# Kernel tuning notes

Hardware: AMD Instinct MI355X
Metric: run time of the kernel (lower is better)

## Reference

```python
import jax, jax.numpy as jnp
import numpy as np

B, N, D, H = 2, 2048, 1024, 16
HD = D // H
SCALE = HD ** -0.5


def setup_inputs() -> dict:
    key = jax.random.key(0)
    ks = jax.random.split(key, 5)
    s = 0.02
    return {
        "x": jax.random.normal(ks[0], (B, N, D), dtype=jnp.float32),
        "Wq": jax.random.normal(ks[1], (D, D), dtype=jnp.float32) * s,
        "Wk": jax.random.normal(ks[2], (D, D), dtype=jnp.float32) * s,
        "Wv": jax.random.normal(ks[3], (D, D), dtype=jnp.float32) * s,
        "Wo": jax.random.normal(ks[4], (D, D), dtype=jnp.float32) * s,
        "bo": jnp.zeros((D,), dtype=jnp.float32),
    }


def reference(x, Wq, Wk, Wv, Wo, bo):
    # Q/K/V projections (torch Linear: y = x @ W.T), bias-free
    q = jnp.einsum("bnd,ed->bne", x, Wq)
    k = jnp.einsum("bnd,ed->bne", x, Wk)
    v = jnp.einsum("bnd,ed->bne", x, Wv)
    # split heads: (b, n, h*d) -> (b, h, n, d)
    split = lambda t: t.reshape(B, N, H, HD).transpose(0, 2, 1, 3)
    q, k, v = split(q), split(k), split(v)
    # full attention matrix, softmax over keys
    sim = jnp.einsum("bhnd,bhmd->bhnm", q, k) * SCALE
    attn = jax.nn.softmax(sim, axis=-1)
    out = jnp.einsum("bhnm,bhmd->bhnd", attn, v)
    out = out.transpose(0, 2, 1, 3).reshape(B, N, D)
    return jnp.einsum("bnd,ed->bne", out, Wo) + bo
```

## Files before the change

### kernel.cpp

```cpp
#include <hip/hip_runtime.h>
#include <hip/hip_bf16.h>
#include <stdint.h>

#define B_ 2
#define N_ 2048
#define D_ 1024
#define H_ 16
#define SCALE_L2E 0.18033688011112042f

typedef unsigned short u16;
typedef unsigned int u32;
using f32x4  = __attribute__((ext_vector_type(4))) float;
using f32x16 = __attribute__((ext_vector_type(16))) float;
using bf16x8 = __attribute__((ext_vector_type(8))) short;
using i16x8  = __attribute__((ext_vector_type(8))) short;

__device__ __forceinline__ u16 f2b(float f) {
  unsigned u = __float_as_uint(f);
  return (u16)((u + 0x7FFFu + ((u >> 16) & 1u)) >> 16);
}
__device__ __forceinline__ u32 pk2(float lo, float hi) {
  u32 r;
  asm("v_cvt_pk_bf16_f32 %0, %1, %2" : "=v"(r) : "v"(lo), "v"(hi));
  return r;
}
__device__ __forceinline__ float ex2(float x) {
  return __builtin_amdgcn_exp2f(x);
}
__device__ __forceinline__ void async16(const u16* g, u16* l) {
  __builtin_amdgcn_global_load_lds(
      (const __attribute__((address_space(1))) void*)g,
      (__attribute__((address_space(3))) void*)l, 16, 0, 0);
}
__device__ __forceinline__ void cfence() {
  asm volatile("" ::: "memory");
  __builtin_amdgcn_sched_barrier(0);
}

__global__ __launch_bounds__(256) void cast_all(
    const float* __restrict__ x, const float* __restrict__ w0,
    const float* __restrict__ w1, const float* __restrict__ w2,
    const float* __restrict__ w3, u16* __restrict__ xb, u16* __restrict__ Wb) {
  const int i = (blockIdx.x * 256 + threadIdx.x) * 8;
  const float* s;
  u16* d;
  if (i < 4194304) { s = x + i; d = xb + i; }
  else {
    const int j = i - 4194304;
    const int wsel = j >> 20;
    const float* w = wsel == 0 ? w0 : wsel == 1 ? w1 : wsel == 2 ? w2 : w3;
    s = w + (j & 1048575);
    d = Wb + j;
  }
  union { u32 u[4]; i16x8 v; } o;
#pragma unroll
  for (int j = 0; j < 4; ++j) o.u[j] = pk2(s[2 * j], s[2 * j + 1]);
  *(i16x8*)d = o.v;
}

template <int F32OUT>
__global__ __launch_bounds__(256) void gemm_bt(
    const u16* __restrict__ A, const u16* __restrict__ Bt,
    void* __restrict__ C0, size_t sCz, const float* __restrict__ bias,
    int M, int Nn, int K) {
  __shared__ __align__(16) u16 As[128 * 64];
  __shared__ __align__(16) u16 Bs[64 * 64];
  const int tid = threadIdx.x;
  const int w = tid >> 6, l = tid & 63;
  const int wm = w >> 1, wn = w & 1;
  const int la = l & 15, lb = l >> 4;
  const int tM = blockIdx.y * 128, tN = blockIdx.x * 64;

  const int srow8 = l >> 3;
  const int scol  = ((l & 7) ^ srow8) << 3;
  const u16* gA = A + (size_t)(tM + w * 32 + srow8) * K + scol;
  const u16* gB = Bt + (size_t)(tN + w * 16 + srow8) * K + scol;
  u16* lA = As + w * 2048;
  u16* lB = Bs + w * 1024;

  f32x4 acc[4][2] = {};

  for (int k0 = 0; k0 < K; k0 += 64) {
#pragma unroll
    for (int c = 0; c < 4; ++c)
      async16(gA + (size_t)(c * 8) * K, lA + c * 512);
#pragma unroll
    for (int c = 0; c < 2; ++c)
      async16(gB + (size_t)(c * 8) * K, lB + c * 512);
    gA += 64; gB += 64;
    __syncthreads();
    bf16x8 af[4][2], bfr[2][2];
#pragma unroll
    for (int i = 0; i < 4; ++i) {
      const int row = wm * 64 + i * 16 + la;
#pragma unroll
      for (int kk = 0; kk < 2; ++kk)
        af[i][kk] = *(const bf16x8*)(As + row * 64 + (((kk * 4 + lb) ^ (row & 7)) << 3));
    }
#pragma unroll
    for (int j = 0; j < 2; ++j) {
      const int row = wn * 32 + j * 16 + la;
#pragma unroll
      for (int kk = 0; kk < 2; ++kk)
        bfr[j][kk] = *(const bf16x8*)(Bs + row * 64 + (((kk * 4 + lb) ^ (row & 7)) << 3));
    }
#pragma unroll
    for (int kk = 0; kk < 2; ++kk)
#pragma unroll
      for (int i = 0; i < 4; ++i)
#pragma unroll
        for (int j = 0; j < 2; ++j)
          acc[i][j] = __builtin_amdgcn_mfma_f32_16x16x32_bf16(
              af[i][kk], bfr[j][kk], acc[i][j], 0, 0, 0);
    __syncthreads();
  }

  const int zsel = F32OUT ? 0 : (tN >> 10);
  const int tNl = F32OUT ? tN : (tN & 1023);
  const float osc = (!F32OUT && zsel == 0) ? SCALE_L2E : 1.0f;
  const int ld = F32OUT ? Nn : 1024;
#pragma unroll
  for (int i = 0; i < 4; ++i) {
    const int row = tM + wm * 64 + i * 16 + lb * 4;
#pragma unroll
    for (int j = 0; j < 2; ++j) {
      const int col = tNl + wn * 32 + j * 16 + la;
#pragma unroll
      for (int r = 0; r < 4; ++r) {
        const float v = acc[i][j][r];
        if (F32OUT) {
          ((float*)C0)[(size_t)(row + r) * ld + col] = v + bias[col];
        } else {
          (((u16*)C0) + (size_t)zsel * sCz)[(size_t)(row + r) * ld + col] = f2b(v * osc);
        }
      }
    }
  }
}

__global__ __launch_bounds__(256) void vtrans(const u16* __restrict__ V,
                                              u16* __restrict__ Vt) {
  __shared__ u16 T[64][72];
  const int tid = threadIdx.x;
  const int rt = blockIdx.x, h = blockIdx.y;
  const int r = tid >> 3, c = (tid & 7) * 8;
#pragma unroll
  for (int p = 0; p < 2; ++p) {
    i16x8 v = *(const i16x8*)(V + (size_t)(rt * 64 + p * 32 + r) * D_ + h * 64 + c);
#pragma unroll
    for (int j = 0; j < 8; ++j) T[p * 32 + r][c + j] = (u16)v[j];
  }
  __syncthreads();
  const int b = rt >> 5, nb = (rt & 31) * 64;
#pragma unroll
  for (int p = 0; p < 2; ++p) {
    const int d = p * 32 + r;
    i16x8 o;
#pragma unroll
    for (int j = 0; j < 8; ++j) o[j] = (short)T[c + j][d];
    *(i16x8*)(Vt + ((size_t)((b * 16 + h) * 64 + d)) * (size_t)N_ + nb + c) = o;
  }
}

__global__ __launch_bounds__(256) void attn_fused(
    const u16* __restrict__ Q, const u16* __restrict__ Kb,
    const u16* __restrict__ VtG, u16* __restrict__ O) {
  __shared__ __align__(16) u16 Ks[2 * 64 * 64];
  __shared__ __align__(16) u16 Vs[2 * 64 * 64];
  const int tid = threadIdx.x;
  const int w = tid >> 6, l = tid & 63;
  const int q = l & 31, hi = l >> 5;

  const int flat = blockIdx.x + 16 * blockIdx.y;
  const int logical = (flat & 7) * 64 + (flat >> 3);
  const int qx = logical & 15;
  const int y  = logical >> 4;

  const int b = y >> 4, h = y & 15;
  const int q0 = qx * 128 + w * 32;

  const u16* Qrow = Q + (size_t)(b * N_ + q0 + q) * D_ + h * 64;
  bf16x8 qf[4];
#pragma unroll
  for (int s = 0; s < 4; ++s) qf[s] = *(const bf16x8*)(Qrow + s * 16 + hi * 8);

  const int srow = l >> 3;
  const int scol = ((l & 7) ^ srow) << 3;
  const int kprow = w * 16 + (srow & 3) + ((srow & 4) << 1);
  const u16* Kg = Kb + (size_t)(b * N_ + kprow) * D_ + h * 64 + scol;
  const u16* Vg = VtG + (size_t)(y * 64 + w * 16 + srow) * N_ + scol;

  const int qsw = (q & 7) << 3;
  const int qr0 = q * 64, qr1 = (32 + q) * 64;

  union { u32 u[4]; bf16x8 v; } ones;
#pragma unroll
  for (int j = 0; j < 4; ++j) ones.u[j] = 0x3F803F80u;

  f32x16 o0 = {}, o1 = {}, o_l = {};

  auto stage = [&](int t, int buf) {
    const u16* kg = Kg + (size_t)(t * 64) * D_;
    u16* kd = Ks + buf * 4096 + w * 1024;
    async16(kg, kd);
    async16(kg + (size_t)4 * D_, kd + 512);
    const u16* vg = Vg + t * 64;
    u16* vd = Vs + buf * 4096 + w * 1024;
    async16(vg, vd);
    async16(vg + (size_t)8 * N_, vd + 512);
  };

  const int NT = N_ / 64;
  stage(0, 0);
  stage(1, 1);

  for (int t = 0; t < NT; ++t) {
    const int buf = t & 1;
    if (t + 1 < NT) asm volatile("s_waitcnt vmcnt(4)" ::: "memory");
    else            asm volatile("s_waitcnt vmcnt(0)" ::: "memory");
    __builtin_amdgcn_s_barrier();
    cfence();
    const u16* KT = Ks + buf * 4096;
    const u16* VT = Vs + buf * 4096;

    f32x16 p0 = {}, p1 = {};
    __builtin_amdgcn_s_setprio(1);
#pragma unroll
    for (int s = 0; s < 4; ++s) {
      const int off = (s * 16 + hi * 8) ^ qsw;
      bf16x8 kf0 = *(const bf16x8*)(KT + qr0 + off);
      bf16x8 kf1 = *(const bf16x8*)(KT + qr1 + off);
      p0 = __builtin_amdgcn_mfma_f32_32x32x16_bf16(kf0, qf[s], p0, 0, 0, 0);
      p1 = __builtin_amdgcn_mfma_f32_32x32x16_bf16(kf1, qf[s], p1, 0, 0, 0);
    }
    __builtin_amdgcn_s_setprio(0);

#pragma unroll
    for (int r = 0; r < 16; ++r) p0[r] = ex2(p0[r]);
#pragma unroll
    for (int r = 0; r < 16; ++r) p1[r] = ex2(p1[r]);

    __builtin_amdgcn_s_setprio(1);
#pragma unroll
    for (int ks = 0; ks < 4; ++ks) {
      const f32x16& P = (ks < 2) ? p0 : p1;
      const int rbq = (ks & 1) * 8;
      union { u32 u[4]; bf16x8 v; } pb;
#pragma unroll
      for (int j = 0; j < 4; ++j) pb.u[j] = pk2(P[rbq + 2 * j], P[rbq + 2 * j + 1]);
      const int off = (ks * 16 + hi * 8) ^ qsw;
      bf16x8 va0 = *(const bf16x8*)(VT + qr0 + off);
      bf16x8 va1 = *(const bf16x8*)(VT + qr1 + off);
      o0  = __builtin_amdgcn_mfma_f32_32x32x16_bf16(va0, pb.v, o0, 0, 0, 0);
      o1  = __builtin_amdgcn_mfma_f32_32x32x16_bf16(va1, pb.v, o1, 0, 0, 0);
      o_l = __builtin_amdgcn_mfma_f32_32x32x16_bf16(ones.v, pb.v, o_l, 0, 0, 0);
    }
    __builtin_amdgcn_s_setprio(0);
    cfence();
    __builtin_amdgcn_s_barrier();
    cfence();
    if (t + 2 < NT) stage(t + 2, buf);
  }

  const float inv = 1.f / o_l[0];
  u16* Ob = O + (size_t)(b * N_ + q0 + q) * D_ + h * 64;
#pragma unroll
  for (int rh = 0; rh < 4; ++rh) {
    uint2 s0, s1;
    s0.x = pk2(o0[4 * rh + 0] * inv, o0[4 * rh + 1] * inv);
    s0.y = pk2(o0[4 * rh + 2] * inv, o0[4 * rh + 3] * inv);
    s1.x = pk2(o1[4 * rh + 0] * inv, o1[4 * rh + 1] * inv);
    s1.y = pk2(o1[4 * rh + 2] * inv, o1[4 * rh + 3] * inv);
    *(uint2*)(Ob + 8 * rh + 4 * hi)      = s0;
    *(uint2*)(Ob + 32 + 8 * rh + 4 * hi) = s1;
  }
}

extern "C" void kernel_launch(void* const* d_in, const int* in_sizes, int n_in,
                              void* d_out, int out_size, void* d_ws, size_t ws_size,
                              hipStream_t stream) {
  const float* x  = (const float*)d_in[0];
  const float* Wq = (const float*)d_in[1];
  const float* Wk = (const float*)d_in[2];
  const float* Wv = (const float*)d_in[3];
  const float* Wo = (const float*)d_in[4];
  const float* bo = (const float*)d_in[5];
  float* out = (float*)d_out;

  char* ws = (char*)d_ws;
  u16* xb   = (u16*)(ws);
  u16* Wb   = (u16*)(ws + (8ull << 20));
  u16* QKV  = (u16*)(ws + (16ull << 20));
  u16* Ob   = (u16*)(ws + (40ull << 20));
  u16* VtG  = xb;

  cast_all<<<dim3(4096), dim3(256), 0, stream>>>(x, Wq, Wk, Wv, Wo, xb, Wb);

  gemm_bt<0><<<dim3(48, 32), dim3(256), 0, stream>>>(
      xb, Wb, QKV, (size_t)(4096 * 1024), (const float*)nullptr,
      4096, 3072, 1024);

  vtrans<<<dim3(64, 16), dim3(256), 0, stream>>>(QKV + 2 * 4096 * 1024, VtG);

  attn_fused<<<dim3(16, 32), dim3(256), 0, stream>>>(
      QKV, QKV + 4096 * 1024, VtG, Ob);

  gemm_bt<1><<<dim3(16, 32), dim3(256), 0, stream>>>(
      Ob, Wb + 3 * 1048576, out, (size_t)0, bo, 4096, 1024, 1024);
}
```

Baseline: 127.2 us.

## Software-pipeline QK^T ahead of PV in attention and widen GEMM N-tile

The attention loop is restructured so the QK^T MFMAs for the next key tile run while the current tile's exponentials and PV MFMAs execute, using ping-pong score registers. K and V staging are split so K for tile t+2 is issued right after the barrier and V after the PV step, with the waitcnt thresholds adjusted to match. Separately, the bf16 GEMM tile grows from 128x64 to 128x128, halving grid width to improve operand reuse. This costs more registers per thread (double score buffers, 16 accumulators in the GEMM) and more LDS, which may lower occupancy. The smaller GEMM grid (768 and 256 blocks) also reduces parallelism across CUs.

```diff
diff --git a/kernel.cpp b/kernel.cpp
--- a/kernel.cpp
+++ b/kernel.cpp
@@ -64,32 +64,32 @@
     void* __restrict__ C0, size_t sCz, const float* __restrict__ bias,
     int M, int Nn, int K) {
   __shared__ __align__(16) u16 As[128 * 64];
-  __shared__ __align__(16) u16 Bs[64 * 64];
+  __shared__ __align__(16) u16 Bs[128 * 64];
   const int tid = threadIdx.x;
   const int w = tid >> 6, l = tid & 63;
   const int wm = w >> 1, wn = w & 1;
   const int la = l & 15, lb = l >> 4;
-  const int tM = blockIdx.y * 128, tN = blockIdx.x * 64;
+  const int tM = blockIdx.y * 128, tN = blockIdx.x * 128;
 
   const int srow8 = l >> 3;
   const int scol  = ((l & 7) ^ srow8) << 3;
   const u16* gA = A + (size_t)(tM + w * 32 + srow8) * K + scol;
-  const u16* gB = Bt + (size_t)(tN + w * 16 + srow8) * K + scol;
+  const u16* gB = Bt + (size_t)(tN + w * 32 + srow8) * K + scol;
   u16* lA = As + w * 2048;
-  u16* lB = Bs + w * 1024;
-
-  f32x4 acc[4][2] = {};
+  u16* lB = Bs + w * 2048;
+
+  f32x4 acc[4][4] = {};
 
   for (int k0 = 0; k0 < K; k0 += 64) {
 #pragma unroll
     for (int c = 0; c < 4; ++c)
       async16(gA + (size_t)(c * 8) * K, lA + c * 512);
 #pragma unroll
-    for (int c = 0; c < 2; ++c)
+    for (int c = 0; c < 4; ++c)
       async16(gB + (size_t)(c * 8) * K, lB + c * 512);
     gA += 64; gB += 64;
     __syncthreads();
-    bf16x8 af[4][2], bfr[2][2];
+    bf16x8 af[4][2], bfr[4][2];
 #pragma unroll
     for (int i = 0; i < 4; ++i) {
       const int row = wm * 64 + i * 16 + la;
@@ -98,8 +98,8 @@
         af[i][kk] = *(const bf16x8*)(As + row * 64 + (((kk * 4 + lb) ^ (row & 7)) << 3));
     }
 #pragma unroll
-    for (int j = 0; j < 2; ++j) {
-      const int row = wn * 32 + j * 16 + la;
+    for (int j = 0; j < 4; ++j) {
+      const int row = wn * 64 + j * 16 + la;
 #pragma unroll
       for (int kk = 0; kk < 2; ++kk)
         bfr[j][kk] = *(const bf16x8*)(Bs + row * 64 + (((kk * 4 + lb) ^ (row & 7)) << 3));
@@ -109,7 +109,7 @@
 #pragma unroll
       for (int i = 0; i < 4; ++i)
 #pragma unroll
-        for (int j = 0; j < 2; ++j)
+        for (int j = 0; j < 4; ++j)
           acc[i][j] = __builtin_amdgcn_mfma_f32_16x16x32_bf16(
               af[i][kk], bfr[j][kk], acc[i][j], 0, 0, 0);
     __syncthreads();
@@ -123,8 +123,8 @@
   for (int i = 0; i < 4; ++i) {
     const int row = tM + wm * 64 + i * 16 + lb * 4;
 #pragma unroll
-    for (int j = 0; j < 2; ++j) {
-      const int col = tNl + wn * 32 + j * 16 + la;
+    for (int j = 0; j < 4; ++j) {
+      const int col = tNl + wn * 64 + j * 16 + la;
 #pragma unroll
       for (int r = 0; r < 4; ++r) {
         const float v = acc[i][j][r];
@@ -198,56 +198,56 @@
   for (int j = 0; j < 4; ++j) ones.u[j] = 0x3F803F80u;
 
   f32x16 o0 = {}, o1 = {}, o_l = {};
-
-  auto stage = [&](int t, int buf) {
+  const int NT = N_ / 64;
+
+  auto stageK = [&](int t, int buf) {
     const u16* kg = Kg + (size_t)(t * 64) * D_;
     u16* kd = Ks + buf * 4096 + w * 1024;
     async16(kg, kd);
     async16(kg + (size_t)4 * D_, kd + 512);
+  };
+  auto stageV = [&](int t, int buf) {
     const u16* vg = Vg + t * 64;
     u16* vd = Vs + buf * 4096 + w * 1024;
     async16(vg, vd);
     async16(vg + (size_t)8 * N_, vd + 512);
   };
-
-  const int NT = N_ / 64;
-  stage(0, 0);
-  stage(1, 1);
-
-  for (int t = 0; t < NT; ++t) {
-    const int buf = t & 1;
-    if (t + 1 < NT) asm volatile("s_waitcnt vmcnt(4)" ::: "memory");
-    else            asm volatile("s_waitcnt vmcnt(0)" ::: "memory");
-    __builtin_amdgcn_s_barrier();
-    cfence();
-    const u16* KT = Ks + buf * 4096;
-    const u16* VT = Vs + buf * 4096;
-
-    f32x16 p0 = {}, p1 = {};
+  auto qkt = [&](int u, f32x16& n0, f32x16& n1) {
+    const u16* KT = Ks + (u & 1) * 4096;
+#pragma unroll
+    for (int r = 0; r < 16; ++r) { n0[r] = 0.f; n1[r] = 0.f; }
     __builtin_amdgcn_s_setprio(1);
 #pragma unroll
     for (int s = 0; s < 4; ++s) {
       const int off = (s * 16 + hi * 8) ^ qsw;
       bf16x8 kf0 = *(const bf16x8*)(KT + qr0 + off);
       bf16x8 kf1 = *(const bf16x8*)(KT + qr1 + off);
-      p0 = __builtin_amdgcn_mfma_f32_32x32x16_bf16(kf0, qf[s], p0, 0, 0, 0);
-      p1 = __builtin_amdgcn_mfma_f32_32x32x16_bf16(kf1, qf[s], p1, 0, 0, 0);
+      n0 = __builtin_amdgcn_mfma_f32_32x32x16_bf16(kf0, qf[s], n0, 0, 0, 0);
+      n1 = __builtin_amdgcn_mfma_f32_32x32x16_bf16(kf1, qf[s], n1, 0, 0, 0);
     }
     __builtin_amdgcn_s_setprio(0);
-
-#pragma unroll
-    for (int r = 0; r < 16; ++r) p0[r] = ex2(p0[r]);
-#pragma unroll
-    for (int r = 0; r < 16; ++r) p1[r] = ex2(p1[r]);
-
+  };
+
+  auto body = [&](int u, f32x16& c0, f32x16& c1, f32x16& n0, f32x16& n1) {
+    if (u + 1 < NT) asm volatile("s_waitcnt vmcnt(2)" ::: "memory");
+    else            asm volatile("s_waitcnt vmcnt(0)" ::: "memory");
+    __builtin_amdgcn_s_barrier();
+    cfence();
+    if (u + 2 < NT) stageK(u + 2, u & 1);
+    if (u + 1 < NT) qkt(u + 1, n0, n1);
+#pragma unroll
+    for (int r = 0; r < 16; ++r) c0[r] = ex2(c0[r]);
+#pragma unroll
+    for (int r = 0; r < 16; ++r) c1[r] = ex2(c1[r]);
+    const u16* VT = Vs + (u & 1) * 4096;
     __builtin_amdgcn_s_setprio(1);
 #pragma unroll
     for (int ks = 0; ks < 4; ++ks) {
-      const f32x16& P = (ks < 2) ? p0 : p1;
+      const f32x16& P = (ks < 2) ? c0 : c1;
       const int rbq = (ks & 1) * 8;
-      union { u32 u[4]; bf16x8 v; } pb;
-#pragma unroll
-      for (int j = 0; j < 4; ++j) pb.u[j] = pk2(P[rbq + 2 * j], P[rbq + 2 * j + 1]);
+      union { u32 u4[4]; bf16x8 v; } pb;
+#pragma unroll
+      for (int j = 0; j < 4; ++j) pb.u4[j] = pk2(P[rbq + 2 * j], P[rbq + 2 * j + 1]);
       const int off = (ks * 16 + hi * 8) ^ qsw;
       bf16x8 va0 = *(const bf16x8*)(VT + qr0 + off);
       bf16x8 va1 = *(const bf16x8*)(VT + qr1 + off);
@@ -259,7 +259,19 @@
     cfence();
     __builtin_amdgcn_s_barrier();
     cfence();
-    if (t + 2 < NT) stage(t + 2, buf);
+    if (u + 2 < NT) stageV(u + 2, u & 1);
+  };
+
+  stageK(0, 0); stageV(0, 0); stageK(1, 1); stageV(1, 1);
+  asm volatile("s_waitcnt vmcnt(6)" ::: "memory");
+  __builtin_amdgcn_s_barrier();
+  cfence();
+  f32x16 pa0, pa1, pb0, pb1;
+  qkt(0, pa0, pa1);
+
+  for (int t = 0; t < NT; t += 2) {
+    body(t,     pa0, pa1, pb0, pb1);
+    body(t + 1, pb0, pb1, pa0, pa1);
   }
 
   const float inv = 1.f / o_l[0];
@@ -296,7 +308,7 @@
 
   cast_all<<<dim3(4096), dim3(256), 0, stream>>>(x, Wq, Wk, Wv, Wo, xb, Wb);
 
-  gemm_bt<0><<<dim3(48, 32), dim3(256), 0, stream>>>(
+  gemm_bt<0><<<dim3(24, 32), dim3(256), 0, stream>>>(
       xb, Wb, QKV, (size_t)(4096 * 1024), (const float*)nullptr,
       4096, 3072, 1024);
 
@@ -305,6 +317,6 @@
   attn_fused<<<dim3(16, 32), dim3(256), 0, stream>>>(
       QKV, QKV + 4096 * 1024, VtG, Ob);
 
-  gemm_bt<1><<<dim3(16, 32), dim3(256), 0, stream>>>(
+  gemm_bt<1><<<dim3(8, 32), dim3(256), 0, stream>>>(
       Ob, Wb + 3 * 1048576, out, (size_t)0, bo, 4096, 1024, 1024);
 }
```

New measurement: 132.8 us. 1.04x slower.

## Double-buffer LDS tiles in bf16 GEMM with async prefetch two stages ahead

Applied to the files above, without the earlier changes.

Splits the GEMM's shared-memory A/B tiles into two buffers and issues the async global-to-LDS loads for the next tiles while the current tile is multiplied. Explicit vmcnt waits and raw barriers replace the full __syncthreads after every load. The aim is to hide global memory latency behind the MFMA work. In exchange it doubles LDS use per block, which may lower occupancy, and it depends on the hand-counted vmcnt value being correct.

```diff
diff --git a/kernel.cpp b/kernel.cpp
--- a/kernel.cpp
+++ b/kernel.cpp
@@ -63,8 +63,8 @@
     const u16* __restrict__ A, const u16* __restrict__ Bt,
     void* __restrict__ C0, size_t sCz, const float* __restrict__ bias,
     int M, int Nn, int K) {
-  __shared__ __align__(16) u16 As[128 * 64];
-  __shared__ __align__(16) u16 Bs[64 * 64];
+  __shared__ __align__(16) u16 As[2][128 * 64];
+  __shared__ __align__(16) u16 Bs[2][64 * 64];
   const int tid = threadIdx.x;
   const int w = tid >> 6, l = tid & 63;
   const int wm = w >> 1, wn = w & 1;
@@ -75,34 +75,44 @@
   const int scol  = ((l & 7) ^ srow8) << 3;
   const u16* gA = A + (size_t)(tM + w * 32 + srow8) * K + scol;
   const u16* gB = Bt + (size_t)(tN + w * 16 + srow8) * K + scol;
-  u16* lA = As + w * 2048;
-  u16* lB = Bs + w * 1024;
+
+  auto stage = [&](int t, int buf) {
+    const int ko = t * 64;
+    u16* lA = As[buf] + w * 2048;
+    u16* lB = Bs[buf] + w * 1024;
+#pragma unroll
+    for (int c = 0; c < 4; ++c)
+      async16(gA + (size_t)(c * 8) * K + ko, lA + c * 512);
+#pragma unroll
+    for (int c = 0; c < 2; ++c)
+      async16(gB + (size_t)(c * 8) * K + ko, lB + c * 512);
+  };
 
   f32x4 acc[4][2] = {};
-
-  for (int k0 = 0; k0 < K; k0 += 64) {
-#pragma unroll
-    for (int c = 0; c < 4; ++c)
-      async16(gA + (size_t)(c * 8) * K, lA + c * 512);
-#pragma unroll
-    for (int c = 0; c < 2; ++c)
-      async16(gB + (size_t)(c * 8) * K, lB + c * 512);
-    gA += 64; gB += 64;
-    __syncthreads();
+  const int NT = K / 64;
+  stage(0, 0);
+  stage(1, 1);
+
+  for (int t = 0; t < NT; ++t) {
+    const int buf = t & 1;
+    if (t + 1 < NT) asm volatile("s_waitcnt vmcnt(6)" ::: "memory");
+    else            asm volatile("s_waitcnt vmcnt(0)" ::: "memory");
+    __builtin_amdgcn_s_barrier();
+    cfence();
     bf16x8 af[4][2], bfr[2][2];
 #pragma unroll
     for (int i = 0; i < 4; ++i) {
       const int row = wm * 64 + i * 16 + la;
 #pragma unroll
       for (int kk = 0; kk < 2; ++kk)
-        af[i][kk] = *(const bf16x8*)(As + row * 64 + (((kk * 4 + lb) ^ (row & 7)) << 3));
+        af[i][kk] = *(const bf16x8*)(As[buf] + row * 64 + (((kk * 4 + lb) ^ (row & 7)) << 3));
     }
 #pragma unroll
     for (int j = 0; j < 2; ++j) {
       const int row = wn * 32 + j * 16 + la;
 #pragma unroll
       for (int kk = 0; kk < 2; ++kk)
-        bfr[j][kk] = *(const bf16x8*)(Bs + row * 64 + (((kk * 4 + lb) ^ (row & 7)) << 3));
+        bfr[j][kk] = *(const bf16x8*)(Bs[buf] + row * 64 + (((kk * 4 + lb) ^ (row & 7)) << 3));
     }
 #pragma unroll
     for (int kk = 0; kk < 2; ++kk)
@@ -112,7 +122,10 @@
         for (int j = 0; j < 2; ++j)
           acc[i][j] = __builtin_amdgcn_mfma_f32_16x16x32_bf16(
               af[i][kk], bfr[j][kk], acc[i][j], 0, 0, 0);
-    __syncthreads();
+    cfence();
+    __builtin_amdgcn_s_barrier();
+    cfence();
+    if (t + 2 < NT) stage(t + 2, buf);
   }
 
   const int zsel = F32OUT ? 0 : (tN >> 10);
```

New measurement: 118.0 us. 7.2% less time.
